# Kernel tuning notes

Hardware: AMD Instinct MI355X
Metric: run time of the kernel (lower is better)

Reference implementation:

```python
import jax, jax.numpy as jnp
import numpy as np
from jax import lax

B, DZ, H, U, T, V = 256, 512, 512, 16, 16, 512  # batch, latent, lstm hidden, segments, steps/segment, vocab


def setup_inputs() -> dict:
    key = jax.random.key(0)
    ks = jax.random.split(key, 32)
    w = lambda k, shape: jax.random.normal(k, shape, jnp.float32) * 0.05
    d = {
        'z': jax.random.normal(ks[0], (B, DZ), jnp.float32),
        'x': jax.random.randint(ks[1], (B, U * T), 0, V),
        # conductor init-state projection: DZ -> 4H
        'Wc': w(ks[2], (4 * H, DZ)), 'bc': jnp.zeros((4 * H,), jnp.float32),
        # conductor 2-layer LSTM (input H, hidden H)
        'cWih0': w(ks[3], (4 * H, H)), 'cWhh0': w(ks[4], (4 * H, H)),
        'cbih0': jnp.zeros((4 * H,), jnp.float32), 'cbhh0': jnp.zeros((4 * H,), jnp.float32),
        'cWih1': w(ks[5], (4 * H, H)), 'cWhh1': w(ks[6], (4 * H, H)),
        'cbih1': jnp.zeros((4 * H,), jnp.float32), 'cbhh1': jnp.zeros((4 * H,), jnp.float32),
        # decoder init-state projection: H -> 4H
        'Wd': w(ks[7], (4 * H, H)), 'bd': jnp.zeros((4 * H,), jnp.float32),
        # decoder 2-layer LSTM (layer0 input 2H, layer1 input H, hidden H)
        'dWih0': w(ks[8], (4 * H, 2 * H)), 'dWhh0': w(ks[9], (4 * H, H)),
        'dbih0': jnp.zeros((4 * H,), jnp.float32), 'dbhh0': jnp.zeros((4 * H,), jnp.float32),
        'dWih1': w(ks[10], (4 * H, H)), 'dWhh1': w(ks[11], (4 * H, H)),
        'dbih1': jnp.zeros((4 * H,), jnp.float32), 'dbhh1': jnp.zeros((4 * H,), jnp.float32),
        # token embedding and output distribution head
        'emb': w(ks[12], (V, H)),
        'Wo': w(ks[13], (V, H)), 'bo': jnp.zeros((V,), jnp.float32),
    }
    return d


def _cell(x, h, c, Wih, Whh, bih, bhh):
    # PyTorch LSTM gate order: i, f, g, o
    g = x @ Wih.T + bih + h @ Whh.T + bhh
    i, f, gg, o = jnp.split(g, 4, axis=-1)
    c = jax.nn.sigmoid(f) * c + jax.nn.sigmoid(i) * jnp.tanh(gg)
    h = jax.nn.sigmoid(o) * jnp.tanh(c)
    return h, c


def _lstm_layer(xp, h0, c0, Whh, bhh):
    # xp: [N, T, 4H] = precomputed x @ Wih.T + bih
    def step(carry, xg):
        h, c = carry
        g = xg + h @ Whh.T + bhh
        i, f, gg, o = jnp.split(g, 4, axis=-1)
        c = jax.nn.sigmoid(f) * c + jax.nn.sigmoid(i) * jnp.tanh(gg)
        h = jax.nn.sigmoid(o) * jnp.tanh(c)
        return (h, c), h
    _, ys = lax.scan(step, (h0, c0), jnp.swapaxes(xp, 0, 1))
    return jnp.swapaxes(ys, 0, 1)  # [N, T, H]


def reference(z, x, Wc, bc, cWih0, cWhh0, cbih0, cbhh0, cWih1, cWhh1, cbih1, cbhh1,
              Wd, bd, dWih0, dWhh0, dbih0, dbhh0, dWih1, dWhh1, dbih1, dbhh1,
              emb, Wo, bo):
    Bz = z.shape[0]
    # --- conductor ---
    ci = jnp.tanh(z @ Wc.T + bc)  # [B, 4H]
    h1, h2, c1, c2 = ci[:, :H], ci[:, H:2 * H], ci[:, 2 * H:3 * H], ci[:, 3 * H:]
    o0 = jnp.zeros((Bz, H), ci.dtype)

    def cstep(carry, _):
        o, h1, c1, h2, c2 = carry
        h1, c1 = _cell(o, h1, c1, cWih0, cWhh0, cbih0, cbhh0)
        h2, c2 = _cell(h1, h2, c2, cWih1, cWhh1, cbih1, cbhh1)
        return (h2, h1, c1, h2, c2), h2

    _, couts = lax.scan(cstep, (o0, h1, c1, h2, c2), None, length=U)
    cond_out = jnp.swapaxes(couts, 0, 1)  # [B, U, H]

    # --- decoder init states ---
    states = jnp.tanh(cond_out @ Wd.T + bd).reshape(Bz * U, 4 * H)
    dh1, dh2, dc1, dc2 = (states[:, :H], states[:, H:2 * H],
                          states[:, 2 * H:3 * H], states[:, 3 * H:])
    h_init = dh1 + dh2  # [BU, H]

    # --- teacher-forced decoder ---
    xt = x.reshape(Bz * U, T)
    e = emb[xt]  # [BU, T, H]
    e = jnp.concatenate([jnp.zeros((Bz * U, 1, H), e.dtype), e[:, :-1]], axis=1)
    inp = jnp.concatenate(
        [e, jnp.broadcast_to(h_init[:, None], (Bz * U, T, H))], axis=-1)  # [BU, T, 2H]

    y0 = _lstm_layer(inp @ dWih0.T + dbih0, dh1, dc1, dWhh0, dbhh0)
    y1 = _lstm_layer(y0 @ dWih1.T + dbih1, dh2, dc2, dWhh1, dbhh1)
    dist = jax.nn.softmax(y1 @ Wo.T + bo, axis=-1)  # [BU, T, V]
    return dist.reshape(Bz, U * T, V)
```

## Files before the change

kernel.cpp:

```cpp
#include <hip/hip_runtime.h>
#include <math.h>

#define AS1 __attribute__((address_space(1)))
#define AS3 __attribute__((address_space(3)))

typedef __attribute__((ext_vector_type(8))) short short8v;
typedef __attribute__((ext_vector_type(16))) float f32x16;

constexpr size_t PA4c = (size_t)4096 * 512;
constexpr size_t PABc = (size_t)256 * 512;

__device__ __forceinline__ float sigmoidf_(float x) { return 1.f / (1.f + expf(-x)); }
__device__ __forceinline__ unsigned int f2bfu(float f) {
    unsigned int u = __float_as_uint(f);
    return (u + 0x7FFF + ((u >> 16) & 1)) >> 16;
}
__device__ __forceinline__ float bf2f(unsigned int s) { return __uint_as_float(s << 16); }
__device__ __forceinline__ unsigned int pack2(float v) {
    unsigned int b0 = f2bfu(v);
    unsigned int b1 = f2bfu(v - bf2f(b0));
    return b0 | (b1 << 16);
}
__device__ __forceinline__ float unpack2(unsigned int p) { return bf2f(p & 0xffffu) + bf2f(p >> 16); }

__device__ __forceinline__ void xswz(int d, int ngx, int ngy, int& bx, int& by) {
    int nwg = ngx * ngy;
    int q = nwg >> 3, r = nwg & 7, xcd = d & 7, pos = d >> 3;
    int logical = (xcd < r ? xcd * (q + 1) : r * (q + 1) + (xcd - r) * q) + pos;
    bx = logical % ngx; by = logical / ngx;
}

__device__ __forceinline__ size_t offf(int m, int k) {
    return ((size_t)((m >> 5) * 64 + (k >> 3))) * 256 + (size_t)((m & 31) * 8 + (k & 7));
}

template<int N>
__device__ __forceinline__ void wait_vm() {
    asm volatile("s_waitcnt vmcnt(%0) lgkmcnt(0)" :: "n"(N) : "memory");
}

template<int FM, int FN>
__device__ __forceinline__ void gemm_core(
    const short* __restrict__ A1, const short* __restrict__ B1,
    const short* __restrict__ A2, const short* __restrict__ B2,
    int M, int N, int nsteps, int pairSwitch,
    int bx, int by, short* lds, f32x16 (&acc)[FM][FN])
{
    constexpr int ABLK = 4 * FM, BBLK = 2 * FN;
    constexpr int ACH = 2 * ABLK * 2, BCH = 2 * BBLK * 2;
    constexpr int CHT = ACH + BCH;
    constexpr int CPW = CHT / 8;
    constexpr int NBUF = 3;
    constexpr int BUFSH = CHT * 512;
    const int tid = threadIdx.x, lane = tid & 63, wid = tid >> 6;
    const int wm = wid >> 1, wn = wid & 1;
    const int l31 = lane & 31, loct = lane >> 5;
    const int mblk0 = by * ABLK, nblk0 = bx * BBLK;
    const size_t planeA = (size_t)M * 512, planeB = (size_t)N * 512;

    const short* cur[CPW];
    const short* nxt[CPW];
    int ldo[CPW];
    #pragma unroll
    for (int i = 0; i < CPW; ++i) {
        int c = wid * CPW + i;
        ldo[i] = c * 512;
        size_t off;
        const short *b1, *b2;
        if (c < ACH) {
            int plane = c / (ABLK * 2), rem = c % (ABLK * 2), blk = rem >> 1, piece = rem & 1;
            off = (size_t)plane * planeA + (size_t)(mblk0 + blk) * 16384 + piece * 512 + lane * 8;
            b1 = A1; b2 = A2;
        } else {
            int cb = c - ACH;
            int plane = cb / (BBLK * 2), rem = cb % (BBLK * 2), blk = rem >> 1, piece = rem & 1;
            off = (size_t)plane * planeB + (size_t)(nblk0 + blk) * 16384 + piece * 512 + lane * 8;
            b1 = B1; b2 = B2;
        }
        cur[i] = b1 + off;
        nxt[i] = b2 ? (b2 + off) : (b1 + off);
    }

    #pragma unroll
    for (int fm = 0; fm < FM; ++fm)
        #pragma unroll
        for (int fn = 0; fn < FN; ++fn)
            acc[fm][fn] = (f32x16){};

    auto STAGE = [&](int bufIdx) {
        short* db = lds + bufIdx * BUFSH;
        #pragma unroll
        for (int i = 0; i < CPW; ++i) {
            __builtin_amdgcn_global_load_lds((const AS1 unsigned int*)cur[i],
                                             (AS3 unsigned int*)(db + ldo[i]), 16, 0, 0);
            cur[i] += 1024;
        }
    };

    STAGE(0); STAGE(1);
    wait_vm<CPW>();
    __builtin_amdgcn_s_barrier();

    for (int t = 0; t < nsteps; ++t) {
        int s = t + NBUF - 1;
        if (s < nsteps) {
            if (s == pairSwitch) {
                #pragma unroll
                for (int i = 0; i < CPW; ++i) cur[i] = nxt[i];
            }
            STAGE(s % NBUF);
        }
        const short* L = lds + (t % NBUF) * BUFSH;
        #pragma unroll
        for (int ksub = 0; ksub < 2; ++ksub) {
            short8v a[FM][2], b[FN][2];
            #pragma unroll
            for (int p = 0; p < 2; ++p) {
                #pragma unroll
                for (int f = 0; f < FM; ++f)
                    a[f][p] = *(const short8v*)(L + (p * (ABLK * 2) + (wm * FM + f) * 2 + ksub) * 512
                                                  + loct * 256 + l31 * 8);
                #pragma unroll
                for (int f = 0; f < FN; ++f)
                    b[f][p] = *(const short8v*)(L + (ACH + p * (BBLK * 2) + (wn * FN + f) * 2 + ksub) * 512
                                                  + loct * 256 + l31 * 8);
            }
            #pragma unroll
            for (int pp = 0; pp < 3; ++pp) {
                const int pa = (pp == 2) ? 1 : 0, pb = (pp == 1) ? 1 : 0;
                #pragma unroll
                for (int fm = 0; fm < FM; ++fm)
                    #pragma unroll
                    for (int fn = 0; fn < FN; ++fn)
                        acc[fm][fn] = __builtin_amdgcn_mfma_f32_32x32x16_bf16(
                            a[fm][pa], b[fn][pb], acc[fm][fn], 0, 0, 0);
            }
        }
        if (t + 2 < nsteps) wait_vm<CPW>();
        else                wait_vm<0>();
        __builtin_amdgcn_s_barrier();
    }
}

template<int FM, int FN>
__device__ __forceinline__ void epi_f32(f32x16 (&acc)[FM][FN], int bx, int by, int N,
                                        float* __restrict__ Cout, const float* __restrict__ bias, int act)
{
    constexpr int ROWS = 128 * FM, COLS = 64 * FN;
    const int tid = threadIdx.x, lane = tid & 63, wid = tid >> 6;
    const int wm = wid >> 1, wn = wid & 1, l31 = lane & 31, loct = lane >> 5;
    #pragma unroll
    for (int fm = 0; fm < FM; ++fm)
        #pragma unroll
        for (int fn = 0; fn < FN; ++fn) {
            int col = bx * COLS + wn * FN * 32 + fn * 32 + l31;
            int rb  = by * ROWS + wm * FM * 32 + fm * 32 + 4 * loct;
            #pragma unroll
            for (int reg = 0; reg < 16; ++reg) {
                int row = rb + (reg & 3) + 8 * (reg >> 2);
                float xv = acc[fm][fn][reg] + (bias ? bias[row] : 0.f);
                if (act) xv = tanhf(xv);
                Cout[(size_t)row * N + col] = xv;
            }
        }
}

template<int FM, int FN>
__device__ __forceinline__ void epi_pack(f32x16 (&acc)[FM][FN], int bx, int by, int N,
                                         unsigned int* __restrict__ packOut)
{
    constexpr int ROWS = 128 * FM, COLS = 64 * FN;
    const int tid = threadIdx.x, lane = tid & 63, wid = tid >> 6;
    const int wm = wid >> 1, wn = wid & 1, l31 = lane & 31, loct = lane >> 5;
    uint4* P4 = (uint4*)packOut;
    #pragma unroll
    for (int fm = 0; fm < FM; ++fm)
        #pragma unroll
        for (int fn = 0; fn < FN; ++fn) {
            int col = bx * COLS + wn * FN * 32 + fn * 32 + l31;
            int ub = by * (ROWS / 4) + wm * FM * 8 + fm * 8 + loct;
            #pragma unroll
            for (int ug = 0; ug < 4; ++ug) {
                int u = ub + 2 * ug;
                uint4 v;
                v.x = pack2(acc[fm][fn][4 * ug + 0]);
                v.y = pack2(acc[fm][fn][4 * ug + 1]);
                v.z = pack2(acc[fm][fn][4 * ug + 2]);
                v.w = pack2(acc[fm][fn][4 * ug + 3]);
                P4[(size_t)u * N + col] = v;
            }
        }
}

template<int FM, int FN>
__device__ __forceinline__ void epi_gate2(
    f32x16 (&acc)[FM][FN], int bx, int by, int N, short* hl,
    const float* __restrict__ bab,
    const unsigned int* __restrict__ hgP,
    const unsigned int* __restrict__ embT,
    const int* __restrict__ xidx,
    float* __restrict__ cT,
    short* __restrict__ hout, size_t hps,
    short* __restrict__ condp, int ustep)
{
    constexpr int ABLK = 4 * FM, BBLK = 2 * FN;
    constexpr int ROWS = 32 * ABLK, COLS = 32 * BBLK;
    constexpr int CHN = ABLK * BBLK * 256;
    const int tid = threadIdx.x, lane = tid & 63, wid = tid >> 6;
    const int wm = wid >> 1, wn = wid & 1, l31 = lane & 31, loct = lane >> 5;
    #pragma unroll
    for (int fm = 0; fm < FM; ++fm) {
        #pragma unroll
        for (int fn = 0; fn < FN; ++fn) {
            const int col = bx * COLS + wn * FN * 32 + fn * 32 + l31;
            const int ub = by * (ROWS / 4) + wm * FM * 8 + fm * 8 + loct;
            int tok = -1;
            if (xidx) tok = xidx[(size_t)col * 16];
            uint4 hv[4]; uint4 ev[4]; float cv[4]; float4 bv[4];
            #pragma unroll
            for (int ug = 0; ug < 4; ++ug) {
                int u = ub + 2 * ug;
                bv[ug] = *(const float4*)&bab[4 * u];
                cv[ug] = cT[(size_t)u * N + col];
                if (hgP) hv[ug] = ((const uint4*)hgP)[(size_t)u * N + col];
            }
            if (embT && tok >= 0) {
                #pragma unroll
                for (int ug = 0; ug < 4; ++ug) {
                    int u = ub + 2 * ug;
                    ev[ug] = ((const uint4*)embT)[(size_t)u * 512 + tok];
                }
            }
            #pragma unroll
            for (int ug = 0; ug < 4; ++ug) {
                int u = ub + 2 * ug;
                float gi = acc[fm][fn][4 * ug + 0] + bv[ug].x;
                float gf = acc[fm][fn][4 * ug + 1] + bv[ug].y;
                float gg = acc[fm][fn][4 * ug + 2] + bv[ug].z;
                float go = acc[fm][fn][4 * ug + 3] + bv[ug].w;
                if (hgP) {
                    gi += unpack2(hv[ug].x); gf += unpack2(hv[ug].y);
                    gg += unpack2(hv[ug].z); go += unpack2(hv[ug].w);
                }
                if (embT && tok >= 0) {
                    gi += unpack2(ev[ug].x); gf += unpack2(ev[ug].y);
                    gg += unpack2(ev[ug].z); go += unpack2(ev[ug].w);
                }
                float c = sigmoidf_(gf) * cv[ug] + sigmoidf_(gi) * tanhf(gg);
                cT[(size_t)u * N + col] = c;
                float h = sigmoidf_(go) * tanhf(c);
                unsigned int p01 = pack2(h);
                int u_loc = wm * FM * 8 + fm * 8 + loct + 2 * ug;
                int m_loc = wn * FN * 32 + fn * 32 + l31;
                int offl = ((m_loc >> 5) * ABLK + (u_loc >> 3)) * 256 + (m_loc & 31) * 8 + (u_loc & 7);
                hl[offl] = (short)(p01 & 0xffffu);
                hl[CHN + offl] = (short)(p01 >> 16);
                if (condp) {
                    int np = col * 16 + ustep;
                    size_t oc = offf(np, u);
                    condp[oc] = (short)(p01 & 0xffffu);
                    condp[PA4c + oc] = (short)(p01 >> 16);
                }
            }
        }
    }
    __syncthreads();
    constexpr int LB = (ABLK == 8) ? 3 : 2;
    for (int p = 0; p < 2; ++p) {
        for (int jj = tid; jj < CHN / 8; jj += 512) {
            int lc = jj >> 5, m31 = jj & 31;
            int m5 = lc >> LB, u3 = lc & (ABLK - 1);
            size_t gc = (size_t)((bx * BBLK + m5) * 64 + by * ABLK + u3);
            *(short8v*)(hout + p * hps + gc * 256 + m31 * 8) = *(const short8v*)(hl + p * CHN + jj * 8);
        }
    }
}

template<int FM, int FN>
__global__ __launch_bounds__(512, 1) void gemm_packk(
    const short* A1, const short* B1, const short* A2, const short* B2,
    int M, int N, int nsteps, int psw, unsigned int* packOut)
{
    __shared__ __align__(16) short lds[3 * (2 * (4 * FM) * 2 + 2 * (2 * FN) * 2) * 512];
    int d = blockIdx.y * gridDim.x + blockIdx.x;
    int bx, by; xswz(d, gridDim.x, gridDim.y, bx, by);
    f32x16 acc[FM][FN];
    gemm_core<FM, FN>(A1, B1, A2, B2, M, N, nsteps, psw, bx, by, lds, acc);
    epi_pack<FM, FN>(acc, bx, by, N, packOut);
}

template<int FM, int FN>
__global__ __launch_bounds__(512, 1) void gemm_split(
    const short* A1, const short* B1, int M, int N, int nsteps,
    const float* bias, short* hA, short* hB, size_t ps, float* cA, float* cB)
{
    __shared__ __align__(16) short lds[3 * (2 * (4 * FM) * 2 + 2 * (2 * FN) * 2) * 512];
    int d = blockIdx.y * gridDim.x + blockIdx.x;
    int bx, by; xswz(d, gridDim.x, gridDim.y, bx, by);
    f32x16 acc[FM][FN];
    gemm_core<FM, FN>(A1, B1, nullptr, nullptr, M, N, nsteps, 100, bx, by, lds, acc);
    constexpr int ROWS = 128 * FM, COLS = 64 * FN;
    const int tid = threadIdx.x, lane = tid & 63, wid = tid >> 6;
    const int wm = wid >> 1, wn = wid & 1, l31 = lane & 31, loct = lane >> 5;
    #pragma unroll
    for (int fm = 0; fm < FM; ++fm)
        #pragma unroll
        for (int fn = 0; fn < FN; ++fn) {
            int col = bx * COLS + wn * FN * 32 + fn * 32 + l31;
            int rb  = by * ROWS + wm * FM * 32 + fm * 32 + 4 * loct;
            #pragma unroll
            for (int reg = 0; reg < 16; ++reg) {
                int row = rb + (reg & 3) + 8 * (reg >> 2);
                float xv = tanhf(acc[fm][fn][reg] + bias[row]);
                if (row < 1024) {
                    short* hp = (row < 512) ? hA : hB;
                    size_t o = offf(col, row & 511);
                    unsigned int p01 = pack2(xv);
                    hp[o] = (short)(p01 & 0xffffu);
                    hp[ps + o] = (short)(p01 >> 16);
                } else {
                    float* cp = (row < 1536) ? cA : cB;
                    cp[(size_t)(row & 511) * N + col] = xv;
                }
            }
        }
}

__global__ __launch_bounds__(512, 1) void cond_cell(
    const short* A1, const short* B1, const short* A2, const short* B2,
    int nsteps, int psw,
    const float* bab, float* cT,
    short* hout, short* condp, int ustep)
{
    __shared__ __align__(16) short lds[3 * 24 * 512];
    int d = blockIdx.y * gridDim.x + blockIdx.x;
    int bx, by; xswz(d, gridDim.x, gridDim.y, bx, by);
    f32x16 acc[1][1];
    gemm_core<1, 1>(A1, B1, A2, B2, 2048, 256, nsteps, psw, bx, by, lds, acc);
    epi_gate2<1, 1>(acc, bx, by, 256, lds, bab, nullptr, nullptr, nullptr,
                    cT, hout, PABc, condp, ustep);
}

struct DecArgs {
    const short *dWhh0P, *dWih1P, *dWhh1P, *WoP;
    const float *babd0, *babd1, *bo;
    const unsigned int *hgP, *embT;
    const int* x;
    float *c0T, *c1dT;
    short *h0a, *h0b, *h1da, *h1db;
    float *LgA, *LgB;
    float* out;
    int t;
};

__global__ __launch_bounds__(512, 1) void dec_step(DecArgs A)
{
    __shared__ __align__(16) short lds[3 * 48 * 512];
    const int role = blockIdx.x >> 8;
    const int dd = blockIdx.x & 255;
    const int t = A.t;
    short* h0[2]  = { A.h0a, A.h0b };
    short* h1d[2] = { A.h1da, A.h1db };
    float* Lg[2]  = { A.LgA, A.LgB };

    if (role == 0) {
        if (t <= 15) {
            int pin = t & 1;
            int bx, by; xswz(dd, 32, 8, bx, by);
            f32x16 acc[2][2];
            gemm_core<2, 2>(A.dWhh0P, h0[pin], nullptr, nullptr, 2048, 4096, 16, 100, bx, by, lds, acc);
            epi_gate2<2, 2>(acc, bx, by, 4096, lds, A.babd0, A.hgP,
                            t > 0 ? A.embT : nullptr, t > 0 ? A.x + (t - 1) : nullptr,
                            A.c0T, h0[pin ^ 1], PA4c, nullptr, 0);
            __syncthreads();
        }
        if (t >= 2 && t <= 17) {
            int k = t - 2;
            int bx, by; xswz(dd, 64, 4, bx, by);
            f32x16 acc1[1][1];
            gemm_core<1, 1>(A.WoP, h1d[(k + 1) & 1], nullptr, nullptr, 512, 4096, 16, 100, bx, by, lds, acc1);
            epi_f32<1, 1>(acc1, bx, by, 4096, Lg[k & 1], nullptr, 0);
        }
    } else {
        if (t >= 1 && t <= 16) {
            int s = t - 1;
            int pin2 = s & 1;
            int bx, by; xswz(dd, 32, 8, bx, by);
            f32x16 acc[2][2];
            gemm_core<2, 2>(A.dWih1P, h0[(s + 1) & 1], A.dWhh1P, h1d[pin2],
                            2048, 4096, 32, 16, bx, by, lds, acc);
            epi_gate2<2, 2>(acc, bx, by, 4096, lds, A.babd1, nullptr, nullptr, nullptr,
                            A.c1dT, h1d[pin2 ^ 1], PA4c, nullptr, 0);
            __syncthreads();
        }
        if (t >= 3) {
            int k = t - 3;
            const float* Lsrc = Lg[k & 1];
            float* tile = (float*)lds;
            float* red  = (float*)lds + 16 * 513;
            float* red2 = red + 512;
            const int tid = threadIdx.x;
            const int mj = tid & 15, vs = tid >> 4;
            const int m = dd * 16 + mj;
            float lv[16];
            #pragma unroll
            for (int i = 0; i < 16; ++i) {
                int v = vs * 16 + i;
                lv[i] = Lsrc[(size_t)v * 4096 + m] + A.bo[v];
            }
            float mx = lv[0];
            #pragma unroll
            for (int i = 1; i < 16; ++i) mx = fmaxf(mx, lv[i]);
            red[vs * 16 + mj] = mx;
            __syncthreads();
            for (int o = 16; o >= 1; o >>= 1) {
                if (vs < o) red[vs * 16 + mj] = fmaxf(red[vs * 16 + mj], red[(vs + o) * 16 + mj]);
                __syncthreads();
            }
            mx = red[mj];
            float sum = 0.f;
            #pragma unroll
            for (int i = 0; i < 16; ++i) {
                float e = expf(lv[i] - mx);
                sum += e;
                tile[mj * 513 + vs * 16 + i] = e;
            }
            red2[vs * 16 + mj] = sum;
            __syncthreads();
            for (int o = 16; o >= 1; o >>= 1) {
                if (vs < o) red2[vs * 16 + mj] += red2[(vs + o) * 16 + mj];
                __syncthreads();
            }
            const int r = tid >> 5, c = tid & 31;
            float invr = 1.f / red2[r];
            for (int kk = 0; kk < 16; ++kk) {
                int v = kk * 32 + c;
                A.out[((size_t)(dd * 16 + r) * 16 + k) * 512 + v] = tile[r * 513 + v] * invr;
            }
        }
    }
}

struct PrepEnt { const float* src; const float* src2; void* dst; int ldw, col0, perm, total, op; };
struct PrepArgs { PrepEnt e[18]; int n; };

__global__ void prep_all(PrepArgs pa)
{
    for (int ei = 0; ei < pa.n; ++ei) {
        PrepEnt E = pa.e[ei];
        for (int o = blockIdx.x * 256 + threadIdx.x; o < E.total; o += gridDim.x * 256) {
            if (E.op == 0) {
                int c = o >> 8, w = o & 255, r = w >> 3, jj = w & 7;
                int n = (c >> 6) * 32 + r, k = (c & 63) * 8 + jj;
                int nsrc = E.perm ? ((n >> 2) + 512 * (n & 3)) : n;
                float v = E.src[(size_t)nsrc * E.ldw + E.col0 + k];
                unsigned int b0 = f2bfu(v);
                short* pl = (short*)E.dst;
                pl[o] = (short)b0;
                pl[E.total + o] = (short)f2bfu(v - bf2f(b0));
            } else {
                int src = (o >> 2) + 512 * (o & 3);
                ((float*)E.dst)[o] = E.src[src] + E.src2[src];
            }
        }
    }
}

extern "C" void kernel_launch(void* const* d_in, const int* in_sizes, int n_in,
                              void* d_out, int out_size, void* d_ws, size_t ws_size,
                              hipStream_t stream)
{
    const float* z     = (const float*)d_in[0];
    const int*   x     = (const int*)  d_in[1];
    const float* Wc    = (const float*)d_in[2];
    const float* bc    = (const float*)d_in[3];
    const float* cWih0 = (const float*)d_in[4];
    const float* cWhh0 = (const float*)d_in[5];
    const float* cbih0 = (const float*)d_in[6];
    const float* cbhh0 = (const float*)d_in[7];
    const float* cWih1 = (const float*)d_in[8];
    const float* cWhh1 = (const float*)d_in[9];
    const float* cbih1 = (const float*)d_in[10];
    const float* cbhh1 = (const float*)d_in[11];
    const float* Wd    = (const float*)d_in[12];
    const float* bd    = (const float*)d_in[13];
    const float* dWih0 = (const float*)d_in[14];
    const float* dWhh0 = (const float*)d_in[15];
    const float* dbih0 = (const float*)d_in[16];
    const float* dbhh0 = (const float*)d_in[17];
    const float* dWih1 = (const float*)d_in[18];
    const float* dWhh1 = (const float*)d_in[19];
    const float* dbih1 = (const float*)d_in[20];
    const float* dbhh1 = (const float*)d_in[21];
    const float* emb   = (const float*)d_in[22];
    const float* Wo    = (const float*)d_in[23];
    const float* bo    = (const float*)d_in[24];
    float* out = (float*)d_out;
    (void)in_sizes; (void)n_in; (void)out_size; (void)ws_size;

    char* wsb = (char*)d_ws;
    size_t off = 0;
    auto alloc = [&](size_t bytes) -> void* {
        off = (off + 255) & ~(size_t)255;
        void* p = wsb + off;
        off += bytes;
        return p;
    };
    const size_t PW  = (size_t)2048 * 512;
    const size_t PWo = (size_t)512 * 512;

    short* WcP    = (short*)alloc(2 * PW * 2);
    short* WdP    = (short*)alloc(2 * PW * 2);
    short* dW1P   = (short*)alloc(2 * PW * 2);
    short* dW2P   = (short*)alloc(2 * PW * 2);
    short* cWih0P = (short*)alloc(2 * PW * 2);
    short* cWhh0P = (short*)alloc(2 * PW * 2);
    short* cWih1P = (short*)alloc(2 * PW * 2);
    short* cWhh1P = (short*)alloc(2 * PW * 2);
    short* dWhh0P = (short*)alloc(2 * PW * 2);
    short* dWih1P = (short*)alloc(2 * PW * 2);
    short* dWhh1P = (short*)alloc(2 * PW * 2);
    short* WoP    = (short*)alloc(2 * PWo * 2);
    short* zpl    = (short*)alloc(2 * PABc * 2);
    short* embpl  = (short*)alloc(2 * PWo * 2);
    float* babc0  = (float*)alloc(2048 * 4);
    float* babc1  = (float*)alloc(2048 * 4);
    float* babd0  = (float*)alloc(2048 * 4);
    float* babd1  = (float*)alloc(2048 * 4);
    float* GbufT  = (float*)alloc((size_t)2048 * 4096 * 4);
    unsigned int* hinitgP = (unsigned int*)alloc((size_t)512 * 4096 * 4 * 4);
    unsigned int* embW0P  = (unsigned int*)alloc((size_t)512 * 512 * 4 * 4);
    short* h1pl[2]; short* h2pl[2];
    h1pl[0] = (short*)alloc(2 * PABc * 2);  h1pl[1] = (short*)alloc(2 * PABc * 2);
    h2pl[0] = (short*)alloc(2 * PABc * 2);  h2pl[1] = (short*)alloc(2 * PABc * 2);
    float* c1T = (float*)alloc((size_t)512 * 256 * 4);
    float* c2T = (float*)alloc((size_t)512 * 256 * 4);
    short* condpl = (short*)alloc(2 * PA4c * 2);
    short* h0pl[2];  short* h1dpl[2];
    h0pl[0]  = (short*)alloc(2 * PA4c * 2); h0pl[1]  = (short*)alloc(2 * PA4c * 2);
    h1dpl[0] = (short*)alloc(2 * PA4c * 2); h1dpl[1] = (short*)alloc(2 * PA4c * 2);
    float* c0T  = (float*)alloc((size_t)512 * 4096 * 4);
    float* c1dT = (float*)alloc((size_t)512 * 4096 * 4);

    float* Lg[2] = { GbufT, GbufT + (size_t)512 * 4096 };

    PrepArgs pa; pa.n = 18;
    auto W8 = [](const float* s, void* d, int ldw, int col0, int perm, int total) {
        PrepEnt e; e.src = s; e.src2 = nullptr; e.dst = d; e.ldw = ldw; e.col0 = col0;
        e.perm = perm; e.total = total; e.op = 0; return e;
    };
    auto B8 = [](const float* a, const float* b, void* d) {
        PrepEnt e; e.src = a; e.src2 = b; e.dst = d; e.ldw = 0; e.col0 = 0;
        e.perm = 0; e.total = 2048; e.op = 1; return e;
    };
    pa.e[0]  = W8(Wc,    WcP,    512,  0,   0, 2048 * 512);
    pa.e[1]  = W8(Wd,    WdP,    512,  0,   0, 2048 * 512);
    pa.e[2]  = W8(dWih0, dW1P,   1024, 0,   1, 2048 * 512);
    pa.e[3]  = W8(dWih0, dW2P,   1024, 512, 1, 2048 * 512);
    pa.e[4]  = W8(cWih0, cWih0P, 512,  0,   1, 2048 * 512);
    pa.e[5]  = W8(cWhh0, cWhh0P, 512,  0,   1, 2048 * 512);
    pa.e[6]  = W8(cWih1, cWih1P, 512,  0,   1, 2048 * 512);
    pa.e[7]  = W8(cWhh1, cWhh1P, 512,  0,   1, 2048 * 512);
    pa.e[8]  = W8(dWhh0, dWhh0P, 512,  0,   1, 2048 * 512);
    pa.e[9]  = W8(dWih1, dWih1P, 512,  0,   1, 2048 * 512);
    pa.e[10] = W8(dWhh1, dWhh1P, 512,  0,   1, 2048 * 512);
    pa.e[11] = W8(Wo,    WoP,    512,  0,   0, 512 * 512);
    pa.e[12] = W8(z,     zpl,    512,  0,   0, 256 * 512);
    pa.e[13] = W8(emb,   embpl,  512,  0,   0, 512 * 512);
    pa.e[14] = B8(cbih0, cbhh0, babc0);
    pa.e[15] = B8(cbih1, cbhh1, babc1);
    pa.e[16] = B8(dbih0, dbhh0, babd0);
    pa.e[17] = B8(dbih1, dbhh1, babd1);
    prep_all<<<dim3(1024), dim3(256), 0, stream>>>(pa);

    gemm_split<2, 2><<<dim3(2, 8), dim3(512), 0, stream>>>(
        WcP, zpl, 2048, 256, 16, bc, h1pl[0], h2pl[0], PABc, c1T, c2T);

    gemm_packk<2, 2><<<dim3(4, 8), dim3(512), 0, stream>>>(
        dW1P, embpl, nullptr, nullptr, 2048, 512, 16, 100, embW0P);

    for (int u = 0; u < 16; ++u) {
        int pin = u & 1;
        if (u == 0)
            cond_cell<<<dim3(4, 16), dim3(512), 0, stream>>>(
                cWhh0P, h1pl[0], nullptr, nullptr, 16, 100,
                babc0, c1T, h1pl[1], nullptr, 0);
        else
            cond_cell<<<dim3(4, 16), dim3(512), 0, stream>>>(
                cWih0P, h2pl[pin], cWhh0P, h1pl[pin], 32, 16,
                babc0, c1T, h1pl[pin ^ 1], nullptr, 0);
        cond_cell<<<dim3(4, 16), dim3(512), 0, stream>>>(
            cWih1P, h1pl[pin ^ 1], cWhh1P, h2pl[pin], 32, 16,
            babc1, c2T, h2pl[pin ^ 1], condpl, u);
    }

    gemm_split<2, 2><<<dim3(32, 8), dim3(512), 0, stream>>>(
        WdP, condpl, 2048, 4096, 16, bd, h0pl[0], h1dpl[0], PA4c, c0T, c1dT);

    gemm_packk<2, 2><<<dim3(32, 8), dim3(512), 0, stream>>>(
        dW2P, h0pl[0], dW2P, h1dpl[0], 2048, 4096, 32, 16, hinitgP);

    for (int t = 0; t <= 18; ++t) {
        DecArgs A;
        A.dWhh0P = dWhh0P; A.dWih1P = dWih1P; A.dWhh1P = dWhh1P; A.WoP = WoP;
        A.babd0 = babd0; A.babd1 = babd1; A.bo = bo;
        A.hgP = hinitgP; A.embT = embW0P; A.x = x;
        A.c0T = c0T; A.c1dT = c1dT;
        A.h0a = h0pl[0]; A.h0b = h0pl[1]; A.h1da = h1dpl[0]; A.h1db = h1dpl[1];
        A.LgA = Lg[0]; A.LgB = Lg[1];
        A.out = out; A.t = t;
        dec_step<<<dim3(512), dim3(512), 0, stream>>>(A);
    }
}
```

Baseline: 2.402 ms.

## Fold h_init gate term into layer-0 recurrent GEMM and halve K-step tiles

Drops the separate precomputed h_init·W gate buffer (hinitgP, a packed-K GEMM before the decoder loop). A cheap plane_add kernel now forms h_init = dh1+dh2 as split-bf16 planes, and each decoder layer-0 step concatenates that term into its recurrent GEMM as a second operand pair. A new gemm_core16 uses 16-wide K chunks with twice as many pipeline steps, which halves the LDS staging buffer so dec_step's shared memory shrinks. The aim is to avoid reading a large fp32 gate buffer every step, at the cost of extra MFMA work per step and more, smaller pipeline iterations.

```diff
diff --git a/kernel.cpp b/kernel.cpp
--- a/kernel.cpp
+++ b/kernel.cpp
@@ -135,6 +135,104 @@
                         acc[fm][fn] = __builtin_amdgcn_mfma_f32_32x32x16_bf16(
                             a[fm][pa], b[fn][pb], acc[fm][fn], 0, 0, 0);
             }
+        }
+        if (t + 2 < nsteps) wait_vm<CPW>();
+        else                wait_vm<0>();
+        __builtin_amdgcn_s_barrier();
+    }
+}
+
+template<int FM, int FN>
+__device__ __forceinline__ void gemm_core16(
+    const short* __restrict__ A1, const short* __restrict__ B1,
+    const short* __restrict__ A2, const short* __restrict__ B2,
+    int M, int N, int nsteps, int pairSwitch,
+    int bx, int by, short* lds, f32x16 (&acc)[FM][FN])
+{
+    constexpr int ABLK = 4 * FM, BBLK = 2 * FN;
+    constexpr int ACH = 2 * ABLK;
+    constexpr int CHT = ACH + 2 * BBLK;
+    constexpr int CPW = CHT / 8;
+    constexpr int NBUF = 3;
+    constexpr int BUFSH = CHT * 512;
+    const int tid = threadIdx.x, lane = tid & 63, wid = tid >> 6;
+    const int wm = wid >> 1, wn = wid & 1;
+    const int l31 = lane & 31, loct = lane >> 5;
+    const int mblk0 = by * ABLK, nblk0 = bx * BBLK;
+    const size_t planeA = (size_t)M * 512, planeB = (size_t)N * 512;
+
+    const short* cur[CPW];
+    const short* nxt[CPW];
+    int ldo[CPW];
+    #pragma unroll
+    for (int i = 0; i < CPW; ++i) {
+        int c = wid * CPW + i;
+        ldo[i] = c * 512;
+        size_t off;
+        const short *b1, *b2;
+        if (c < ACH) {
+            int plane = c / ABLK, blk = c % ABLK;
+            off = (size_t)plane * planeA + (size_t)(mblk0 + blk) * 16384 + lane * 8;
+            b1 = A1; b2 = A2;
+        } else {
+            int cb = c - ACH;
+            int plane = cb / BBLK, blk = cb % BBLK;
+            off = (size_t)plane * planeB + (size_t)(nblk0 + blk) * 16384 + lane * 8;
+            b1 = B1; b2 = B2;
+        }
+        cur[i] = b1 + off;
+        nxt[i] = b2 ? (b2 + off) : (b1 + off);
+    }
+
+    #pragma unroll
+    for (int fm = 0; fm < FM; ++fm)
+        #pragma unroll
+        for (int fn = 0; fn < FN; ++fn)
+            acc[fm][fn] = (f32x16){};
+
+    auto STAGE = [&](int bufIdx) {
+        short* db = lds + bufIdx * BUFSH;
+        #pragma unroll
+        for (int i = 0; i < CPW; ++i) {
+            __builtin_amdgcn_global_load_lds((const AS1 unsigned int*)cur[i],
+                                             (AS3 unsigned int*)(db + ldo[i]), 16, 0, 0);
+            cur[i] += 512;
+        }
+    };
+
+    STAGE(0); STAGE(1);
+    wait_vm<CPW>();
+    __builtin_amdgcn_s_barrier();
+
+    for (int t = 0; t < nsteps; ++t) {
+        int s = t + NBUF - 1;
+        if (s < nsteps) {
+            if (s == pairSwitch) {
+                #pragma unroll
+                for (int i = 0; i < CPW; ++i) cur[i] = nxt[i];
+            }
+            STAGE(s % NBUF);
+        }
+        const short* L = lds + (t % NBUF) * BUFSH;
+        short8v a[FM][2], b[FN][2];
+        #pragma unroll
+        for (int p = 0; p < 2; ++p) {
+            #pragma unroll
+            for (int f = 0; f < FM; ++f)
+                a[f][p] = *(const short8v*)(L + (p * ABLK + wm * FM + f) * 512 + loct * 256 + l31 * 8);
+            #pragma unroll
+            for (int f = 0; f < FN; ++f)
+                b[f][p] = *(const short8v*)(L + (ACH + p * BBLK + wn * FN + f) * 512 + loct * 256 + l31 * 8);
+        }
+        #pragma unroll
+        for (int pp = 0; pp < 3; ++pp) {
+            const int pa = (pp == 2) ? 1 : 0, pb = (pp == 1) ? 1 : 0;
+            #pragma unroll
+            for (int fm = 0; fm < FM; ++fm)
+                #pragma unroll
+                for (int fn = 0; fn < FN; ++fn)
+                    acc[fm][fn] = __builtin_amdgcn_mfma_f32_32x32x16_bf16(
+                        a[fm][pa], b[fn][pb], acc[fm][fn], 0, 0, 0);
         }
         if (t + 2 < nsteps) wait_vm<CPW>();
         else                wait_vm<0>();
@@ -326,6 +424,29 @@
         }
 }
 
+__global__ void plane_add(const short* __restrict__ a, const short* __restrict__ b,
+                          short* __restrict__ o)
+{
+    int n8 = (int)(PA4c / 8);
+    for (int i = blockIdx.x * 256 + threadIdx.x; i < n8; i += gridDim.x * 256) {
+        short8v ah = ((const short8v*)a)[i];
+        short8v al = ((const short8v*)(a + PA4c))[i];
+        short8v bh = ((const short8v*)b)[i];
+        short8v bl = ((const short8v*)(b + PA4c))[i];
+        short8v oh, ol;
+        #pragma unroll
+        for (int j = 0; j < 8; ++j) {
+            float v = bf2f((unsigned short)ah[j]) + bf2f((unsigned short)al[j])
+                    + bf2f((unsigned short)bh[j]) + bf2f((unsigned short)bl[j]);
+            unsigned int p = pack2(v);
+            oh[j] = (short)(p & 0xffffu);
+            ol[j] = (short)(p >> 16);
+        }
+        ((short8v*)o)[i] = oh;
+        ((short8v*)(o + PA4c))[i] = ol;
+    }
+}
+
 __global__ __launch_bounds__(512, 1) void cond_cell(
     const short* A1, const short* B1, const short* A2, const short* B2,
     int nsteps, int psw,
@@ -342,9 +463,9 @@
 }
 
 struct DecArgs {
-    const short *dWhh0P, *dWih1P, *dWhh1P, *WoP;
+    const short *dWhh0P, *dW2P, *dWih1P, *dWhh1P, *WoP, *hiP;
     const float *babd0, *babd1, *bo;
-    const unsigned int *hgP, *embT;
+    const unsigned int *embT;
     const int* x;
     float *c0T, *c1dT;
     short *h0a, *h0b, *h1da, *h1db;
@@ -355,7 +476,7 @@
 
 __global__ __launch_bounds__(512, 1) void dec_step(DecArgs A)
 {
-    __shared__ __align__(16) short lds[3 * 48 * 512];
+    __shared__ __align__(16) short lds[3 * 24 * 512];
     const int role = blockIdx.x >> 8;
     const int dd = blockIdx.x & 255;
     const int t = A.t;
@@ -368,8 +489,9 @@
             int pin = t & 1;
             int bx, by; xswz(dd, 32, 8, bx, by);
             f32x16 acc[2][2];
-            gemm_core<2, 2>(A.dWhh0P, h0[pin], nullptr, nullptr, 2048, 4096, 16, 100, bx, by, lds, acc);
-            epi_gate2<2, 2>(acc, bx, by, 4096, lds, A.babd0, A.hgP,
+            gemm_core16<2, 2>(A.dWhh0P, h0[pin], A.dW2P, A.hiP,
+                              2048, 4096, 64, 32, bx, by, lds, acc);
+            epi_gate2<2, 2>(acc, bx, by, 4096, lds, A.babd0, nullptr,
                             t > 0 ? A.embT : nullptr, t > 0 ? A.x + (t - 1) : nullptr,
                             A.c0T, h0[pin ^ 1], PA4c, nullptr, 0);
             __syncthreads();
@@ -387,8 +509,8 @@
             int pin2 = s & 1;
             int bx, by; xswz(dd, 32, 8, bx, by);
             f32x16 acc[2][2];
-            gemm_core<2, 2>(A.dWih1P, h0[(s + 1) & 1], A.dWhh1P, h1d[pin2],
-                            2048, 4096, 32, 16, bx, by, lds, acc);
+            gemm_core16<2, 2>(A.dWih1P, h0[(s + 1) & 1], A.dWhh1P, h1d[pin2],
+                              2048, 4096, 64, 32, bx, by, lds, acc);
             epi_gate2<2, 2>(acc, bx, by, 4096, lds, A.babd1, nullptr, nullptr, nullptr,
                             A.c1dT, h1d[pin2 ^ 1], PA4c, nullptr, 0);
             __syncthreads();
@@ -528,8 +650,8 @@
     float* babd0  = (float*)alloc(2048 * 4);
     float* babd1  = (float*)alloc(2048 * 4);
     float* GbufT  = (float*)alloc((size_t)2048 * 4096 * 4);
-    unsigned int* hinitgP = (unsigned int*)alloc((size_t)512 * 4096 * 4 * 4);
-    unsigned int* embW0P  = (unsigned int*)alloc((size_t)512 * 512 * 4 * 4);
+    unsigned int* embW0P = (unsigned int*)alloc((size_t)512 * 512 * 4 * 4);
+    short* hipl   = (short*)alloc(2 * PA4c * 2);
     short* h1pl[2]; short* h2pl[2];
     h1pl[0] = (short*)alloc(2 * PABc * 2);  h1pl[1] = (short*)alloc(2 * PABc * 2);
     h2pl[0] = (short*)alloc(2 * PABc * 2);  h2pl[1] = (short*)alloc(2 * PABc * 2);
@@ -597,14 +719,14 @@
     gemm_split<2, 2><<<dim3(32, 8), dim3(512), 0, stream>>>(
         WdP, condpl, 2048, 4096, 16, bd, h0pl[0], h1dpl[0], PA4c, c0T, c1dT);
 
-    gemm_packk<2, 2><<<dim3(32, 8), dim3(512), 0, stream>>>(
-        dW2P, h0pl[0], dW2P, h1dpl[0], 2048, 4096, 32, 16, hinitgP);
+    plane_add<<<dim3(1024), dim3(256), 0, stream>>>(h0pl[0], h1dpl[0], hipl);
 
     for (int t = 0; t <= 18; ++t) {
         DecArgs A;
-        A.dWhh0P = dWhh0P; A.dWih1P = dWih1P; A.dWhh1P = dWhh1P; A.WoP = WoP;
+        A.dWhh0P = dWhh0P; A.dW2P = dW2P; A.dWih1P = dWih1P; A.dWhh1P = dWhh1P;
+        A.WoP = WoP; A.hiP = hipl;
         A.babd0 = babd0; A.babd1 = babd1; A.bo = bo;
-        A.hgP = hinitgP; A.embT = embW0P; A.x = x;
+        A.embT = embW0P; A.x = x;
         A.c0T = c0T; A.c1dT = c1dT;
         A.h0a = h0pl[0]; A.h0b = h0pl[1]; A.h1da = h1dpl[0]; A.h1db = h1dpl[1];
         A.LgA = Lg[0]; A.LgB = Lg[1];
```

Measured after the change: 2.796 ms. 1.16x slower.
